# Optimization experiments

Measured on AMD Instinct MI355X. Metric: run time of the kernel, lower is better.

Reference implementation:

```python
import jax, jax.numpy as jnp
import numpy as np

# Static problem sizes (uniform T/taus make the ragged edge list static).
B, N, F, T, TAU, S = 8, 384, 64, 192, 192, 5
SINK_SHIFT = T                    # min sink index == T (sinks are the new nodes)
N_SINK, N_SOURCE = TAU, T + TAU - 1


def _edge_indices():
    # tril_indices(T+tau, offset=-1), keep sink >= T  (window=None)
    r, c = np.tril_indices(T + TAU, k=-1)
    m = r >= T
    r, c = r[m], c[m]
    e = r.shape[0]
    batch = np.repeat(np.arange(B), e)
    return (jnp.asarray(batch, jnp.int32),
            jnp.asarray(np.tile(r, B), jnp.int32),
            jnp.asarray(np.tile(c, B), jnp.int32))


def setup_inputs() -> dict:
    key = jax.random.key(0)
    ks = jax.random.split(key, 6)
    batch_idx, sink_idx, source_idx = _edge_indices()
    s1, s2 = 1.0 / np.sqrt(2 * F), 1.0 / np.sqrt(F)
    return {
        "nodes": jax.random.normal(ks[0], (B, N, F), jnp.float32),
        "w1": jax.random.uniform(ks[1], (2 * F, F), jnp.float32, -s1, s1),
        "b1": jnp.zeros((F,), jnp.float32),
        "g1": jnp.ones((F,), jnp.float32),
        "be1": jnp.zeros((F,), jnp.float32),
        "w2": jax.random.uniform(ks[2], (F, F), jnp.float32, -s2, s2),
        "b2": jnp.zeros((F,), jnp.float32),
        "g2": jnp.ones((F,), jnp.float32),
        "be2": jnp.zeros((F,), jnp.float32),
        "w3": jax.random.uniform(ks[3], (F, 1), jnp.float32, -s2, s2),
        "b3": jnp.zeros((1,), jnp.float32),
        "gumbel": jax.random.gumbel(ks[4], (S, B, N_SINK, N_SOURCE), jnp.float32),
        "batch_idx": batch_idx,
        "sink_idx": sink_idx,
        "source_idx": source_idx,
    }


def _ln(x, g, b):
    mu = x.mean(-1, keepdims=True)
    v = ((x - mu) ** 2).mean(-1, keepdims=True)
    return (x - mu) * jax.lax.rsqrt(v + 1e-5) * g + b


def reference(nodes, w1, b1, g1, be1, w2, b2, g2, be2, w3, b3,
              gumbel, batch_idx, sink_idx, source_idx):
    # gather sink/source node pairs: [E, 2F]
    sink = nodes[batch_idx, sink_idx]
    src = nodes[batch_idx, source_idx]
    x = jnp.concatenate([sink, src], axis=-1)
    # edge MLP -> per-edge logit
    h = _ln(jax.nn.relu(x @ w1 + b1), g1, be1)
    h = _ln(jax.nn.relu(h @ w2 + b2), g2, be2)
    logits = (h @ w3 + b3)[:, 0]                     # [E]
    # dense-padded grid filled with finfo.min (as in torch)
    neg = jnp.finfo(jnp.float32).min
    gs = jnp.full((B, N_SINK, N_SOURCE), neg, jnp.float32)
    gs = gs.at[batch_idx, sink_idx - SINK_SHIFT, source_idx].set(logits)
    # hard gumbel-softmax over source dim, S independent samples
    y_soft = jax.nn.softmax(gs[None] + gumbel, axis=-1)      # [S,B,192,383]
    y_hard = jax.nn.one_hot(jnp.argmax(y_soft, -1), N_SOURCE, dtype=y_soft.dtype)
    y = y_soft + jax.lax.stop_gradient(y_hard - y_soft)
    e = y.sum(0)
    # straight-through binarize: forward (e>0), backward identity
    e = e + jax.lax.stop_gradient((e > 0).astype(e.dtype) - e)
    valid = e[batch_idx, sink_idx - SINK_SHIFT, source_idx]
    vals = jnp.where(valid > 0, valid, 0.0)
    # dense equivalent of the sparse COO adjacency (B, N, N)
    return jnp.zeros((B, N, N), jnp.float32).at[batch_idx, sink_idx, source_idx].set(vals)
```

## Files before the change

kernel.cpp:

```cpp
#include <hip/hip_runtime.h>
#include <math.h>
#include <stdint.h>

#define BB 8
#define NN 384
#define FF 64
#define TT 192
#define NSRC 383
#define NSINK 192
#define SS 5
#define NEDGE 441600
#define BN (BB * NN)
#define TILE_E 256
#define NBLKE (NEDGE / TILE_E)
#define OUTV ((BB * NN * NN) / 4)

typedef _Float16 half8 __attribute__((ext_vector_type(8)));
typedef __fp16 fp16x2 __attribute__((ext_vector_type(2)));
typedef float floatx4 __attribute__((ext_vector_type(4)));

static __device__ __forceinline__ void split_f16(float x, uint16_t& h, uint16_t& l) {
  const _Float16 hh = (_Float16)x;
  const float hb = (float)hh;
  const _Float16 ll = (_Float16)((x - hb) * 512.f);
  h = __builtin_bit_cast(uint16_t, hh);
  l = __builtin_bit_cast(uint16_t, ll);
}

static __device__ __forceinline__ void split_pair(float x0, float x1,
                                                  uint32_t& hi, uint32_t& lo) {
  const fp16x2 h = __builtin_amdgcn_cvt_pkrtz(x0, x1);
  const float hb0 = (float)h.x, hb1 = (float)h.y;
  const fp16x2 l = __builtin_amdgcn_cvt_pkrtz((x0 - hb0) * 512.f, (x1 - hb1) * 512.f);
  hi = __builtin_bit_cast(uint32_t, h);
  lo = __builtin_bit_cast(uint32_t, l);
}

__global__ __launch_bounds__(64) void prep_all(
    const float* __restrict__ nodes, const float* __restrict__ w1,
    const float* __restrict__ b1,
    const float* __restrict__ w2, const float* __restrict__ b2,
    const float* __restrict__ g1, const float* __restrict__ be1,
    const float* __restrict__ g2, const float* __restrict__ be2,
    const float* __restrict__ w3, const float* __restrict__ b3,
    float* __restrict__ A, float* __restrict__ Bv,
    unsigned short* __restrict__ Whg, unsigned short* __restrict__ Wlg,
    float* __restrict__ wcol, float* __restrict__ cb,
    float* __restrict__ gw, float* __restrict__ cwsgw) {
  const int blk = blockIdx.x;
  const int k = threadIdx.x;
  if (blk < BN / 4) {
    const int bn0 = blk * 4;
    __shared__ float nd[4][FF];
#pragma unroll
    for (int i = 0; i < 4; ++i) nd[i][k] = nodes[(bn0 + i) * FF + k];
    __syncthreads();
    const float bk = b1[k];
    float a0 = bk, a1 = bk, a2 = bk, a3 = bk;
    float q0 = 0.f, q1 = 0.f, q2 = 0.f, q3 = 0.f;
#pragma unroll 8
    for (int f = 0; f < FF; ++f) {
      const float wt = w1[f * FF + k];
      const float wb = w1[(FF + f) * FF + k];
      const float n0 = nd[0][f], n1 = nd[1][f], n2 = nd[2][f], n3 = nd[3][f];
      a0 = fmaf(n0, wt, a0); a1 = fmaf(n1, wt, a1);
      a2 = fmaf(n2, wt, a2); a3 = fmaf(n3, wt, a3);
      q0 = fmaf(n0, wb, q0); q1 = fmaf(n1, wb, q1);
      q2 = fmaf(n2, wb, q2); q3 = fmaf(n3, wb, q3);
    }
    A[(bn0 + 0) * FF + k] = a0;
    A[(bn0 + 1) * FF + k] = a1;
    A[(bn0 + 2) * FF + k] = a2;
    A[(bn0 + 3) * FF + k] = a3;
    const int f4 = k >> 2, ff = k & 3;
    Bv[(f4 * BN + (bn0 + 0)) * 4 + ff] = q0;
    Bv[(f4 * BN + (bn0 + 1)) * 4 + ff] = q1;
    Bv[(f4 * BN + (bn0 + 2)) * 4 + ff] = q2;
    Bv[(f4 * BN + (bn0 + 3)) * 4 + ff] = q3;
  } else {
    const int j = k;
    const int jt = j >> 4, m = j & 15;
    float cbj = b2[j];
    float wc = 0.f;
    for (int kk = 0; kk < FF; ++kk) {
      const float wraw = w2[kk * FF + j];
      const float w = g1[kk] * wraw;
      wc += w;
      cbj = fmaf(be1[kk], wraw, cbj);
      uint16_t hu, lu;
      split_f16(w, hu, lu);
      const int kc = kk >> 5, qq = (kk >> 3) & 3, jj = kk & 7;
      const int idx = (((jt * 2 + kc) * 4 + qq) * 16 + m) * 8 + jj;
      Whg[idx] = hu;
      Wlg[idx] = lu;
    }
    wcol[j] = wc;
    cb[j] = cbj;
    const float gwj = g2[j] * w3[j];
    gw[j] = gwj;
    __shared__ float sA[FF], sB[FF];
    sA[j] = gwj;
    sB[j] = be2[j] * w3[j];
    __syncthreads();
    if (j == 0) {
      float a = 0.f, bq = 0.f;
      for (int i = 0; i < FF; ++i) { a += sA[i]; bq += sB[i]; }
      cwsgw[0] = b3[0] + bq;
      cwsgw[1] = a;
    }
  }
}

__global__ __launch_bounds__(256, 2) void edge_mlp(
    const float* __restrict__ A, const float* __restrict__ Bv,
    const unsigned short* __restrict__ Whg, const unsigned short* __restrict__ Wlg,
    const float* __restrict__ wcolg, const float* __restrict__ cbg,
    const float* __restrict__ gwg, const float* __restrict__ cwsgw,
    const int* __restrict__ bidx, const int* __restrict__ ridx,
    const int* __restrict__ cidx, float* __restrict__ L,
    float4* __restrict__ outv) {
  __shared__ __align__(16) unsigned short XHs[16384];
  __shared__ __align__(16) unsigned short XLs[16384];

  const int tid = threadIdx.x;
  const int wave = tid >> 6;
  const int lane = tid & 63;
  const int q4 = lane >> 4;
  const int c15 = lane & 15;

  const int gtid = blockIdx.x * 256 + tid;
  if (gtid < OUTV) outv[gtid] = make_float4(0.f, 0.f, 0.f, 0.f);

  const int ge = blockIdx.x * TILE_E + tid;
  const int b = bidx[ge], r = ridx[ge], c = cidx[ge];
  const int et_own = lane >> 4, n_own = lane & 15;
  float mu, rstd;
  {
    const float4* pa = (const float4*)(A + (b * NN + r) * FF);
    const float4* pb4 = (const float4*)Bv;
    const int colB = b * NN + c;
    unsigned short* dh = &XHs[wave * 4096 + n_own * 8];
    unsigned short* dl = &XLs[wave * 4096 + n_own * 8];
    float s = 0.f, q = 0.f;
#pragma unroll
    for (int g = 0; g < 8; ++g) {
      const float4 av0 = pa[2 * g], av1 = pa[2 * g + 1];
      const float4 bv0 = pb4[(2 * g) * BN + colB];
      const float4 bv1 = pb4[(2 * g + 1) * BN + colB];
      const float x0 = fmaxf(av0.x + bv0.x, 0.f);
      const float x1 = fmaxf(av0.y + bv0.y, 0.f);
      const float x2 = fmaxf(av0.z + bv0.z, 0.f);
      const float x3 = fmaxf(av0.w + bv0.w, 0.f);
      const float x4 = fmaxf(av1.x + bv1.x, 0.f);
      const float x5 = fmaxf(av1.y + bv1.y, 0.f);
      const float x6 = fmaxf(av1.z + bv1.z, 0.f);
      const float x7 = fmaxf(av1.w + bv1.w, 0.f);
      s += x0 + x1 + x2 + x3 + x4 + x5 + x6 + x7;
      q = fmaf(x0, x0, q); q = fmaf(x1, x1, q);
      q = fmaf(x2, x2, q); q = fmaf(x3, x3, q);
      q = fmaf(x4, x4, q); q = fmaf(x5, x5, q);
      q = fmaf(x6, x6, q); q = fmaf(x7, x7, q);
      int4 hi4, lo4;
      split_pair(x0, x1, *(uint32_t*)&hi4.x, *(uint32_t*)&lo4.x);
      split_pair(x2, x3, *(uint32_t*)&hi4.y, *(uint32_t*)&lo4.y);
      split_pair(x4, x5, *(uint32_t*)&hi4.z, *(uint32_t*)&lo4.z);
      split_pair(x6, x7, *(uint32_t*)&hi4.w, *(uint32_t*)&lo4.w);
      const int choff = ((et_own * 2 + (g >> 2)) * 4 + (g & 3)) * 128;
      *(int4*)(dh + choff) = hi4;
      *(int4*)(dl + choff) = lo4;
    }
    mu = s * (1.f / FF);
    rstd = 1.f / sqrtf(q * (1.f / FF) - mu * mu + 1e-5f);
  }

  half8 whr[4][2], wlr[4][2];
#pragma unroll
  for (int jt = 0; jt < 4; ++jt)
#pragma unroll
    for (int kc = 0; kc < 2; ++kc) {
      const int woff = ((jt * 2 + kc) * 4 + q4) * 128 + c15 * 8;
      whr[jt][kc] = *(const half8*)&Whg[woff];
      wlr[jt][kc] = *(const half8*)&Wlg[woff];
    }

  floatx4 wc4[4], cb4[4], gw4[4];
#pragma unroll
  for (int jt = 0; jt < 4; ++jt) {
    wc4[jt] = *(const floatx4*)(wcolg + 16 * jt + 4 * q4);
    cb4[jt] = *(const floatx4*)(cbg + 16 * jt + 4 * q4);
    gw4[jt] = *(const floatx4*)(gwg + 16 * jt + 4 * q4);
  }
  const float cw = cwsgw[0], sgw = cwsgw[1];

#pragma unroll
  for (int et = 0; et < 4; ++et) {
    floatx4 acc0[4], acc1[4];
#pragma unroll
    for (int jt = 0; jt < 4; ++jt) {
      acc0[jt] = (floatx4){0.f, 0.f, 0.f, 0.f};
      acc1[jt] = (floatx4){0.f, 0.f, 0.f, 0.f};
    }
#pragma unroll
    for (int kc = 0; kc < 2; ++kc) {
      const int xoff = wave * 4096 + ((et * 2 + kc) * 4 + q4) * 128 + c15 * 8;
      const half8 xh = *(const half8*)&XHs[xoff];
      const half8 xl = *(const half8*)&XLs[xoff];
#pragma unroll
      for (int jt = 0; jt < 4; ++jt) {
        acc0[jt] = __builtin_amdgcn_mfma_f32_16x16x32_f16(whr[jt][kc], xh, acc0[jt], 0, 0, 0);
        acc1[jt] = __builtin_amdgcn_mfma_f32_16x16x32_f16(whr[jt][kc], xl, acc1[jt], 0, 0, 0);
        acc1[jt] = __builtin_amdgcn_mfma_f32_16x16x32_f16(wlr[jt][kc], xh, acc1[jt], 0, 0, 0);
      }
    }
    const int e2 = 16 * et + c15;
    const float mue = __shfl(mu, e2, 64);
    const float rse = __shfl(rstd, e2, 64);
    float s1 = 0.f, s2 = 0.f, s3 = 0.f;
#pragma unroll
    for (int jt = 0; jt < 4; ++jt) {
      const floatx4 t4 = acc0[jt] + acc1[jt] * (1.f / 512.f);
#pragma unroll
      for (int rg = 0; rg < 4; ++rg) {
        const float pre = fmaf(rse, fmaf(-mue, wc4[jt][rg], t4[rg]), cb4[jt][rg]);
        const float tr = fmaxf(pre, 0.f);
        s1 += tr;
        s2 = fmaf(tr, tr, s2);
        s3 = fmaf(tr, gw4[jt][rg], s3);
      }
    }
    s1 += __shfl_xor(s1, 16, 64); s1 += __shfl_xor(s1, 32, 64);
    s2 += __shfl_xor(s2, 16, 64); s2 += __shfl_xor(s2, 32, 64);
    s3 += __shfl_xor(s3, 16, 64); s3 += __shfl_xor(s3, 32, 64);
    const int b2 = __shfl(b, e2, 64);
    const int r2 = __shfl(r, e2, 64);
    const int c2 = __shfl(c, e2, 64);
    if (q4 == 0) {
      const float mu2 = s1 * (1.f / FF);
      const float var2 = s2 * (1.f / FF) - mu2 * mu2;
      const float rstd2 = 1.f / sqrtf(var2 + 1e-5f);
      const float logit = fmaf(rstd2, fmaf(-mu2, sgw, s3), cw);
      L[(b2 * NSINK + (r2 - TT)) * NSRC + c2] = logit;
    }
  }
}

__global__ __launch_bounds__(256) void argmax_scatter(
    const float* __restrict__ L, const float* __restrict__ gum,
    float* __restrict__ out) {
  const int pair = blockIdx.x * 4 + (threadIdx.x >> 6);
  const int lane = threadIdx.x & 63;
  const int row = pair % NSINK;
  const int b = pair / NSINK;
  const int r = row + TT;

  const float* __restrict__ lrow = L + (b * NSINK + row) * NSRC;
  const float* __restrict__ g0 = gum + (b * NSINK + row) * NSRC;
  const int sstr = BB * NSINK * NSRC;

  float bv0 = -INFINITY, bv1 = -INFINITY, bv2 = -INFINITY, bv3 = -INFINITY, bv4 = -INFINITY;
  int bi0 = 0, bi1 = 0, bi2 = 0, bi3 = 0, bi4 = 0;
  for (int cc = lane; cc < r; cc += 64) {
    const float lv = lrow[cc];
    const float v0 = lv + g0[0 * sstr + cc];
    const float v1 = lv + g0[1 * sstr + cc];
    const float v2 = lv + g0[2 * sstr + cc];
    const float v3 = lv + g0[3 * sstr + cc];
    const float v4 = lv + g0[4 * sstr + cc];
    if (v0 > bv0) { bv0 = v0; bi0 = cc; }
    if (v1 > bv1) { bv1 = v1; bi1 = cc; }
    if (v2 > bv2) { bv2 = v2; bi2 = cc; }
    if (v3 > bv3) { bv3 = v3; bi3 = cc; }
    if (v4 > bv4) { bv4 = v4; bi4 = cc; }
  }
#pragma unroll
  for (int off = 32; off > 0; off >>= 1) {
    {
      const float ov = __shfl_xor(bv0, off, 64); const int oi = __shfl_xor(bi0, off, 64);
      if (ov > bv0 || (ov == bv0 && oi < bi0)) { bv0 = ov; bi0 = oi; }
    }
    {
      const float ov = __shfl_xor(bv1, off, 64); const int oi = __shfl_xor(bi1, off, 64);
      if (ov > bv1 || (ov == bv1 && oi < bi1)) { bv1 = ov; bi1 = oi; }
    }
    {
      const float ov = __shfl_xor(bv2, off, 64); const int oi = __shfl_xor(bi2, off, 64);
      if (ov > bv2 || (ov == bv2 && oi < bi2)) { bv2 = ov; bi2 = oi; }
    }
    {
      const float ov = __shfl_xor(bv3, off, 64); const int oi = __shfl_xor(bi3, off, 64);
      if (ov > bv3 || (ov == bv3 && oi < bi3)) { bv3 = ov; bi3 = oi; }
    }
    {
      const float ov = __shfl_xor(bv4, off, 64); const int oi = __shfl_xor(bi4, off, 64);
      if (ov > bv4 || (ov == bv4 && oi < bi4)) { bv4 = ov; bi4 = oi; }
    }
  }
  if (lane == 0) {
    float* __restrict__ orow = out + (b * NN + r) * NN;
    orow[bi0] = 1.0f;
    orow[bi1] = 1.0f;
    orow[bi2] = 1.0f;
    orow[bi3] = 1.0f;
    orow[bi4] = 1.0f;
  }
}

extern "C" void kernel_launch(void* const* d_in, const int* in_sizes, int n_in,
                              void* d_out, int out_size, void* d_ws, size_t ws_size,
                              hipStream_t stream) {
  const float* nodes = (const float*)d_in[0];
  const float* w1 = (const float*)d_in[1];
  const float* b1 = (const float*)d_in[2];
  const float* g1 = (const float*)d_in[3];
  const float* be1 = (const float*)d_in[4];
  const float* w2 = (const float*)d_in[5];
  const float* b2 = (const float*)d_in[6];
  const float* g2 = (const float*)d_in[7];
  const float* be2 = (const float*)d_in[8];
  const float* w3 = (const float*)d_in[9];
  const float* b3 = (const float*)d_in[10];
  const float* gum = (const float*)d_in[11];
  const int* bidx = (const int*)d_in[12];
  const int* ridx = (const int*)d_in[13];
  const int* cidx = (const int*)d_in[14];
  float* out = (float*)d_out;

  float* ws = (float*)d_ws;
  float* A = ws;
  float* Bv = A + BN * FF;
  unsigned short* Whg = (unsigned short*)(ws + 393216);
  unsigned short* Wlg = Whg + 4096;
  float* wcol = ws + 397312;
  float* cb = wcol + FF;
  float* gw = cb + FF;
  float* cwsgw = gw + FF;
  float* L = ws + 397520;
  (void)ws_size; (void)n_in; (void)in_sizes; (void)out_size;

  hipLaunchKernelGGL(prep_all, dim3(BN / 4 + 1), dim3(64), 0, stream,
                     nodes, w1, b1, w2, b2, g1, be1, g2, be2, w3, b3,
                     A, Bv, Whg, Wlg, wcol, cb, gw, cwsgw);
  hipLaunchKernelGGL(edge_mlp, dim3(NBLKE), dim3(256), 0, stream,
                     A, Bv, Whg, Wlg, wcol, cb, gw, cwsgw, bidx, ridx, cidx, L,
                     (float4*)out);
  hipLaunchKernelGGL(argmax_scatter, dim3((BB * NSINK) / 4), dim3(256), 0, stream,
                     L, gum, out);
}
```

Measured before the change: 129.6 us.

## Build MFMA operands in registers and stage weights in LDS

The edge MLP no longer has each thread compute one full edge row and round-trip it through 64 KB of shared memory. Each lane now loads its own 16-feature slice of an edge directly in the MFMA operand layout and reduces the LayerNorm statistics with cross-lane shuffles. The split-f16 weights now live in a small shared buffer that MFMA steps read, rather than staying resident in registers. Occupancy bounds go from 2 to 3 blocks per CU. This trades LDS traffic and register pressure for more shuffles and repeated per-edge weight loads from LDS.

```diff
diff --git a/kernel.cpp b/kernel.cpp
--- a/kernel.cpp
+++ b/kernel.cpp
@@ -18,6 +18,7 @@
 typedef _Float16 half8 __attribute__((ext_vector_type(8)));
 typedef __fp16 fp16x2 __attribute__((ext_vector_type(2)));
 typedef float floatx4 __attribute__((ext_vector_type(4)));
+typedef uint32_t uint4v __attribute__((ext_vector_type(4)));
 
 static __device__ __forceinline__ void split_f16(float x, uint16_t& h, uint16_t& l) {
   const _Float16 hh = (_Float16)x;
@@ -111,7 +112,7 @@
   }
 }
 
-__global__ __launch_bounds__(256, 2) void edge_mlp(
+__global__ __launch_bounds__(256, 3) void edge_mlp(
     const float* __restrict__ A, const float* __restrict__ Bv,
     const unsigned short* __restrict__ Whg, const unsigned short* __restrict__ Wlg,
     const float* __restrict__ wcolg, const float* __restrict__ cbg,
@@ -119,81 +120,98 @@
     const int* __restrict__ bidx, const int* __restrict__ ridx,
     const int* __restrict__ cidx, float* __restrict__ L,
     float4* __restrict__ outv) {
-  __shared__ __align__(16) unsigned short XHs[16384];
-  __shared__ __align__(16) unsigned short XLs[16384];
+  __shared__ __align__(16) unsigned short WhS[4096];
+  __shared__ __align__(16) unsigned short WlS[4096];
 
   const int tid = threadIdx.x;
-  const int wave = tid >> 6;
   const int lane = tid & 63;
-  const int q4 = lane >> 4;
-  const int c15 = lane & 15;
+  const int q = lane >> 4;
+  const int n = lane & 15;
+
+  {
+    const int4* gh = (const int4*)Whg;
+    const int4* gl = (const int4*)Wlg;
+    int4* sh = (int4*)WhS;
+    int4* sl = (int4*)WlS;
+    sh[tid] = gh[tid];
+    sh[tid + 256] = gh[tid + 256];
+    sl[tid] = gl[tid];
+    sl[tid + 256] = gl[tid + 256];
+  }
 
   const int gtid = blockIdx.x * 256 + tid;
   if (gtid < OUTV) outv[gtid] = make_float4(0.f, 0.f, 0.f, 0.f);
 
-  const int ge = blockIdx.x * TILE_E + tid;
-  const int b = bidx[ge], r = ridx[ge], c = cidx[ge];
-  const int et_own = lane >> 4, n_own = lane & 15;
-  float mu, rstd;
-  {
+  const int ebase = blockIdx.x * TILE_E + (tid >> 6) * 64 + n;
+  int eb[4], er[4], ec[4];
+#pragma unroll
+  for (int et = 0; et < 4; ++et) {
+    eb[et] = bidx[ebase + 16 * et];
+    er[et] = ridx[ebase + 16 * et];
+    ec[et] = cidx[ebase + 16 * et];
+  }
+  const float cw = cwsgw[0], sgw = cwsgw[1];
+  const float4* __restrict__ pb4 = (const float4*)Bv;
+
+  __syncthreads();
+
+#pragma unroll
+  for (int et = 0; et < 4; ++et) {
+    const int b = eb[et], r = er[et], c = ec[et];
     const float4* pa = (const float4*)(A + (b * NN + r) * FF);
-    const float4* pb4 = (const float4*)Bv;
     const int colB = b * NN + c;
-    unsigned short* dh = &XHs[wave * 4096 + n_own * 8];
-    unsigned short* dl = &XLs[wave * 4096 + n_own * 8];
-    float s = 0.f, q = 0.f;
-#pragma unroll
-    for (int g = 0; g < 8; ++g) {
-      const float4 av0 = pa[2 * g], av1 = pa[2 * g + 1];
-      const float4 bv0 = pb4[(2 * g) * BN + colB];
-      const float4 bv1 = pb4[(2 * g + 1) * BN + colB];
-      const float x0 = fmaxf(av0.x + bv0.x, 0.f);
-      const float x1 = fmaxf(av0.y + bv0.y, 0.f);
-      const float x2 = fmaxf(av0.z + bv0.z, 0.f);
-      const float x3 = fmaxf(av0.w + bv0.w, 0.f);
-      const float x4 = fmaxf(av1.x + bv1.x, 0.f);
-      const float x5 = fmaxf(av1.y + bv1.y, 0.f);
-      const float x6 = fmaxf(av1.z + bv1.z, 0.f);
-      const float x7 = fmaxf(av1.w + bv1.w, 0.f);
-      s += x0 + x1 + x2 + x3 + x4 + x5 + x6 + x7;
-      q = fmaf(x0, x0, q); q = fmaf(x1, x1, q);
-      q = fmaf(x2, x2, q); q = fmaf(x3, x3, q);
-      q = fmaf(x4, x4, q); q = fmaf(x5, x5, q);
-      q = fmaf(x6, x6, q); q = fmaf(x7, x7, q);
-      int4 hi4, lo4;
-      split_pair(x0, x1, *(uint32_t*)&hi4.x, *(uint32_t*)&lo4.x);
-      split_pair(x2, x3, *(uint32_t*)&hi4.y, *(uint32_t*)&lo4.y);
-      split_pair(x4, x5, *(uint32_t*)&hi4.z, *(uint32_t*)&lo4.z);
-      split_pair(x6, x7, *(uint32_t*)&hi4.w, *(uint32_t*)&lo4.w);
-      const int choff = ((et_own * 2 + (g >> 2)) * 4 + (g & 3)) * 128;
-      *(int4*)(dh + choff) = hi4;
-      *(int4*)(dl + choff) = lo4;
-    }
-    mu = s * (1.f / FF);
-    rstd = 1.f / sqrtf(q * (1.f / FF) - mu * mu + 1e-5f);
-  }
-
-  half8 whr[4][2], wlr[4][2];
-#pragma unroll
-  for (int jt = 0; jt < 4; ++jt)
-#pragma unroll
-    for (int kc = 0; kc < 2; ++kc) {
-      const int woff = ((jt * 2 + kc) * 4 + q4) * 128 + c15 * 8;
-      whr[jt][kc] = *(const half8*)&Whg[woff];
-      wlr[jt][kc] = *(const half8*)&Wlg[woff];
-    }
-
-  floatx4 wc4[4], cb4[4], gw4[4];
-#pragma unroll
-  for (int jt = 0; jt < 4; ++jt) {
-    wc4[jt] = *(const floatx4*)(wcolg + 16 * jt + 4 * q4);
-    cb4[jt] = *(const floatx4*)(cbg + 16 * jt + 4 * q4);
-    gw4[jt] = *(const floatx4*)(gwg + 16 * jt + 4 * q4);
-  }
-  const float cw = cwsgw[0], sgw = cwsgw[1];
-
-#pragma unroll
-  for (int et = 0; et < 4; ++et) {
+    const float4 a0 = pa[2 * q],     a1 = pa[2 * q + 1];
+    const float4 a2 = pa[8 + 2 * q], a3 = pa[8 + 2 * q + 1];
+    const float4 v0 = pb4[(2 * q) * BN + colB];
+    const float4 v1 = pb4[(2 * q + 1) * BN + colB];
+    const float4 v2 = pb4[(8 + 2 * q) * BN + colB];
+    const float4 v3 = pb4[(8 + 2 * q + 1) * BN + colB];
+
+    const float x0 = fmaxf(a0.x + v0.x, 0.f);
+    const float x1 = fmaxf(a0.y + v0.y, 0.f);
+    const float x2 = fmaxf(a0.z + v0.z, 0.f);
+    const float x3 = fmaxf(a0.w + v0.w, 0.f);
+    const float x4 = fmaxf(a1.x + v1.x, 0.f);
+    const float x5 = fmaxf(a1.y + v1.y, 0.f);
+    const float x6 = fmaxf(a1.z + v1.z, 0.f);
+    const float x7 = fmaxf(a1.w + v1.w, 0.f);
+    const float x8 = fmaxf(a2.x + v2.x, 0.f);
+    const float x9 = fmaxf(a2.y + v2.y, 0.f);
+    const float x10 = fmaxf(a2.z + v2.z, 0.f);
+    const float x11 = fmaxf(a2.w + v2.w, 0.f);
+    const float x12 = fmaxf(a3.x + v3.x, 0.f);
+    const float x13 = fmaxf(a3.y + v3.y, 0.f);
+    const float x14 = fmaxf(a3.z + v3.z, 0.f);
+    const float x15 = fmaxf(a3.w + v3.w, 0.f);
+
+    uint32_t h0, l0, h1, l1, h2, l2, h3, l3;
+    split_pair(x0, x1, h0, l0); split_pair(x2, x3, h1, l1);
+    split_pair(x4, x5, h2, l2); split_pair(x6, x7, h3, l3);
+    const uint4v hv0 = {h0, h1, h2, h3}, lv0 = {l0, l1, l2, l3};
+    const half8 xh0 = __builtin_bit_cast(half8, hv0);
+    const half8 xl0 = __builtin_bit_cast(half8, lv0);
+    split_pair(x8, x9, h0, l0);  split_pair(x10, x11, h1, l1);
+    split_pair(x12, x13, h2, l2); split_pair(x14, x15, h3, l3);
+    const uint4v hv1 = {h0, h1, h2, h3}, lv1 = {l0, l1, l2, l3};
+    const half8 xh1 = __builtin_bit_cast(half8, hv1);
+    const half8 xl1 = __builtin_bit_cast(half8, lv1);
+
+    float s = x0 + x1 + x2 + x3 + x4 + x5 + x6 + x7 +
+              x8 + x9 + x10 + x11 + x12 + x13 + x14 + x15;
+    float qa = 0.f;
+    qa = fmaf(x0, x0, qa); qa = fmaf(x1, x1, qa);
+    qa = fmaf(x2, x2, qa); qa = fmaf(x3, x3, qa);
+    qa = fmaf(x4, x4, qa); qa = fmaf(x5, x5, qa);
+    qa = fmaf(x6, x6, qa); qa = fmaf(x7, x7, qa);
+    qa = fmaf(x8, x8, qa); qa = fmaf(x9, x9, qa);
+    qa = fmaf(x10, x10, qa); qa = fmaf(x11, x11, qa);
+    qa = fmaf(x12, x12, qa); qa = fmaf(x13, x13, qa);
+    qa = fmaf(x14, x14, qa); qa = fmaf(x15, x15, qa);
+    s += __shfl_xor(s, 16, 64);  s += __shfl_xor(s, 32, 64);
+    qa += __shfl_xor(qa, 16, 64); qa += __shfl_xor(qa, 32, 64);
+    const float mu = s * (1.f / FF);
+    const float rstd = 1.f / sqrtf(qa * (1.f / FF) - mu * mu + 1e-5f);
+
     floatx4 acc0[4], acc1[4];
 #pragma unroll
     for (int jt = 0; jt < 4; ++jt) {
@@ -202,44 +220,44 @@
     }
 #pragma unroll
     for (int kc = 0; kc < 2; ++kc) {
-      const int xoff = wave * 4096 + ((et * 2 + kc) * 4 + q4) * 128 + c15 * 8;
-      const half8 xh = *(const half8*)&XHs[xoff];
-      const half8 xl = *(const half8*)&XLs[xoff];
+      const half8 xh = kc ? xh1 : xh0;
+      const half8 xl = kc ? xl1 : xl0;
 #pragma unroll
       for (int jt = 0; jt < 4; ++jt) {
-        acc0[jt] = __builtin_amdgcn_mfma_f32_16x16x32_f16(whr[jt][kc], xh, acc0[jt], 0, 0, 0);
-        acc1[jt] = __builtin_amdgcn_mfma_f32_16x16x32_f16(whr[jt][kc], xl, acc1[jt], 0, 0, 0);
-        acc1[jt] = __builtin_amdgcn_mfma_f32_16x16x32_f16(wlr[jt][kc], xh, acc1[jt], 0, 0, 0);
+        const int woff = (((jt * 2 + kc) * 4 + q) * 16 + n) * 8;
+        const half8 wh = *(const half8*)&WhS[woff];
+        const half8 wl = *(const half8*)&WlS[woff];
+        acc0[jt] = __builtin_amdgcn_mfma_f32_16x16x32_f16(wh, xh, acc0[jt], 0, 0, 0);
+        acc1[jt] = __builtin_amdgcn_mfma_f32_16x16x32_f16(wh, xl, acc1[jt], 0, 0, 0);
+        acc1[jt] = __builtin_amdgcn_mfma_f32_16x16x32_f16(wl, xh, acc1[jt], 0, 0, 0);
       }
     }
-    const int e2 = 16 * et + c15;
-    const float mue = __shfl(mu, e2, 64);
-    const float rse = __shfl(rstd, e2, 64);
-    float s1 = 0.f, s2 = 0.f, s3 = 0.f;
+
+    float s1 = 0.f, sq2 = 0.f, s3 = 0.f;
 #pragma unroll
     for (int jt = 0; jt < 4; ++jt) {
+      const floatx4 wc4 = *(const floatx4*)(wcolg + 16 * jt + 4 * q);
+      const floatx4 cb4 = *(const floatx4*)(cbg + 16 * jt + 4 * q);
+      const floatx4 gw4 = *(const floatx4*)(gwg + 16 * jt + 4 * q);
       const floatx4 t4 = acc0[jt] + acc1[jt] * (1.f / 512.f);
 #pragma unroll
       for (int rg = 0; rg < 4; ++rg) {
-        const float pre = fmaf(rse, fmaf(-mue, wc4[jt][rg], t4[rg]), cb4[jt][rg]);
+        const float pre = fmaf(rstd, fmaf(-mu, wc4[rg], t4[rg]), cb4[rg]);
         const float tr = fmaxf(pre, 0.f);
         s1 += tr;
-        s2 = fmaf(tr, tr, s2);
-        s3 = fmaf(tr, gw4[jt][rg], s3);
+        sq2 = fmaf(tr, tr, sq2);
+        s3 = fmaf(tr, gw4[rg], s3);
       }
     }
-    s1 += __shfl_xor(s1, 16, 64); s1 += __shfl_xor(s1, 32, 64);
-    s2 += __shfl_xor(s2, 16, 64); s2 += __shfl_xor(s2, 32, 64);
-    s3 += __shfl_xor(s3, 16, 64); s3 += __shfl_xor(s3, 32, 64);
-    const int b2 = __shfl(b, e2, 64);
-    const int r2 = __shfl(r, e2, 64);
-    const int c2 = __shfl(c, e2, 64);
-    if (q4 == 0) {
+    s1 += __shfl_xor(s1, 16, 64);  s1 += __shfl_xor(s1, 32, 64);
+    sq2 += __shfl_xor(sq2, 16, 64); sq2 += __shfl_xor(sq2, 32, 64);
+    s3 += __shfl_xor(s3, 16, 64);  s3 += __shfl_xor(s3, 32, 64);
+    if (q == 0) {
       const float mu2 = s1 * (1.f / FF);
-      const float var2 = s2 * (1.f / FF) - mu2 * mu2;
+      const float var2 = sq2 * (1.f / FF) - mu2 * mu2;
       const float rstd2 = 1.f / sqrtf(var2 + 1e-5f);
       const float logit = fmaf(rstd2, fmaf(-mu2, sgw, s3), cw);
-      L[(b2 * NSINK + (r2 - TT)) * NSRC + c2] = logit;
+      L[(b * NSINK + (r - TT)) * NSRC + c] = logit;
     }
   }
 }
```

New measurement: 132.1 us. About the same (+1.9%).
